# Performance work log

Measured on AMD Instinct MI355X. Metric: run time of the kernel, lower is better.

The kernel has to match this reference:

```python
import jax, jax.numpy as jnp
import numpy as np

N_STATE = 256   # complex state size n (real state is 2n)
N_IN = 128
BATCH = 16
T_STEPS = 2048
H_STEP = 0.01
EPS = 1e-3
LAM_RE_MIN, LAM_RE_MAX, MAX_PHASE = -5.0, -0.5, 6.283


def setup_inputs() -> dict:
    rng = np.random.default_rng(0)
    n, nu = N_STATE, N_IN
    # trainable params (as in torch __init__)
    u1 = rng.random(n)
    u2 = rng.random(n) * 2.0 - 1.0
    alpha = np.log(-(u1 * (LAM_RE_MAX - LAM_RE_MIN) + LAM_RE_MIN)).astype(np.float32)
    theta = (MAX_PHASE * u2).astype(np.float32)
    B_re = (rng.standard_normal((n, nu)) / np.sqrt(2.0 * nu)).astype(np.float32)
    B_im = (rng.standard_normal((n, nu)) / np.sqrt(2.0 * nu)).astype(np.float32)
    # fixed basis-change buffers: rho (normalized), T_inv, P = rho @ T_inv, Pinv
    H1 = rng.standard_normal((n, n))
    H2 = rng.standard_normal((n, n))
    rho = np.block([[H1, -H2], [H2, H1]])
    rho = rho / np.linalg.norm(rho)
    I = np.eye(n)
    T_inv = (1.0 / np.sqrt(2.0)) * np.block([[I, I], [-1j * I, 1j * I]])
    P = rho.astype(np.complex128) @ T_inv
    Pinv = np.linalg.inv(P)
    key = jax.random.key(0)
    k1, k2 = jax.random.split(key)
    return {
        "xi_init": jax.random.normal(k1, (BATCH, 1, 2 * n), dtype=jnp.float32),
        "u_log": jax.random.normal(k2, (BATCH, T_STEPS, nu), dtype=jnp.float32),
        "alpha": jnp.asarray(alpha),
        "theta": jnp.asarray(theta),
        "B_re": jnp.asarray(B_re),
        "B_im": jnp.asarray(B_im),
        "P_re": jnp.asarray(P.real, dtype=jnp.float32),
        "P_im": jnp.asarray(P.imag, dtype=jnp.float32),
        "Pinv_re": jnp.asarray(Pinv.real, dtype=jnp.float32),
        "Pinv_im": jnp.asarray(Pinv.imag, dtype=jnp.float32),
        "T": T_STEPS,
    }


def reference(xi_init, u_log, alpha, theta, B_re, B_im, P_re, P_im, Pinv_re, Pinv_im, T):
    n = alpha.shape[0]
    lam = (-jnp.exp(alpha) - EPS) + 1j * theta          # (n,) complex64
    Bc = B_re + 1j * B_im                               # (n, nu)
    P = P_re + 1j * P_im                                # (2n, 2n)
    Pinv = Pinv_re + 1j * Pinv_im                       # (2n, 2n)
    xi0 = xi_init[:, 0, :]                              # (B, 2n) real

    def step(xi, u_t):
        # xi: (B, 2n) real state; u_t: (B, nu)
        x_tilde = xi.astype(jnp.complex64) @ Pinv.T     # (B, 2n) complex
        x_bar = x_tilde[:, :n]                          # (B, n)
        x_bar_dot = lam * x_bar + u_t.astype(jnp.complex64) @ Bc.T
        x_tilde_dot = jnp.concatenate([x_bar_dot, jnp.conj(x_bar_dot)], axis=-1)
        x_dot = (x_tilde_dot @ P.T).real                # (B, 2n)
        xi_new = xi + H_STEP * x_dot
        return xi_new, xi_new

    u_seq = jnp.swapaxes(u_log, 0, 1)                   # (T, B, nu)
    _, xs = jax.lax.scan(step, xi0, u_seq)              # (T, B, 2n)
    # torch _sim logs xi_init, then skips xi after t=0, logs xi after t=1..T-1
    x_log = jnp.concatenate([xi0[None], xs[1:]], axis=0)  # (T, B, 2n)
    return jnp.swapaxes(x_log, 0, 1)                    # (B, T, 2n)
```

## Files before the change

kernel.cpp:

```cpp
#include <hip/hip_runtime.h>
#include <hip/hip_bf16.h>
#include <cstddef>
#include <cstdint>

#define N_ST 256
#define TWO_N 512
#define NU 128
#define BATCH 16
#define TSTEPS 2048
#define MTOT (BATCH * TSTEPS)
#define H_STEP 0.01f
#define EPS_V 0.001f
#define NCHUNK 32
#define CHUNKL 64

typedef __attribute__((ext_vector_type(4))) float f32x4;
typedef __attribute__((ext_vector_type(4))) short s16x4;
typedef __attribute__((ext_vector_type(8))) short s16x8;

#define OFF_FPK    0
#define OFF_ZPK    8388608
#define OFF_UPK    16777216
#define OFF_WT     18874368
#define OFF_WF     19005440
#define OFF_D      19038208
#define OFF_XBAR0  19039232
#define OFF_E      19047424

static __device__ __forceinline__ float bf2f(short s) {
    return __uint_as_float(((unsigned)(unsigned short)s) << 16);
}

__global__ __launch_bounds__(256) void prep_mega(
    const float* __restrict__ P_re, const float* __restrict__ P_im,
    const float* __restrict__ B_re, const float* __restrict__ B_im,
    const float* __restrict__ alpha, const float* __restrict__ theta,
    const float* __restrict__ Pinv_re, const float* __restrict__ Pinv_im,
    const float* __restrict__ xi0, const float* __restrict__ u,
    short* __restrict__ Wtpk, short* __restrict__ Wfpk,
    float* __restrict__ dbuf, float* __restrict__ xbar0,
    short* __restrict__ upk)
{
    __shared__ float xs[BATCH * TWO_N];
    int blk = blockIdx.x, tid = threadIdx.x;
    if (blk < 1024) {
        int idx = blk * 256 + tid;
        int j = idx >> 9, c = idx & 511;
        float v;
        if (c < N_ST) v = P_re[j * TWO_N + c] + P_re[j * TWO_N + c + N_ST];
        else          v = P_im[j * TWO_N + c] - P_im[j * TWO_N + c - N_ST];
        __hip_bfloat16 b = __float2bfloat16(v);
        Wtpk[((size_t)(j >> 4) * TWO_N + c) * 16 + (j & 15)] = *(short*)&b;
    } else if (blk < 1280) {
        int idx = (blk - 1024) * 256 + tid;
        int k = idx >> 9, c = idx & 511;
        float v = (c < N_ST) ? B_re[c * NU + k] : B_im[(c - N_ST) * NU + k];
        __hip_bfloat16 b = __float2bfloat16(H_STEP * v);
        Wfpk[((size_t)(c >> 4) * NU + k) * 16 + (c & 15)] = *(short*)&b;
    } else if (blk == 1280) {
        int i = tid;
        float dr = 1.0f + H_STEP * (-expf(alpha[i]) - EPS_V);
        float di = H_STEP * theta[i];
        float pr = 1.0f, pi = 0.0f;
        for (int k = 0; k < CHUNKL; ++k) { float nr = pr * dr - pi * di; pi = pr * di + pi * dr; pr = nr; }
        dbuf[i] = dr; dbuf[N_ST + i] = di; dbuf[2 * N_ST + i] = pr; dbuf[3 * N_ST + i] = pi;
    } else if (blk < 1345) {
#pragma unroll
        for (int q = 0; q < 8; ++q)
            *reinterpret_cast<float4*>(&xs[(q * 256 + tid) * 4]) =
                *reinterpret_cast<const float4*>(&xi0[(q * 256 + tid) * 4]);
        __syncthreads();
        int wv = tid >> 6, l = tid & 63;
        int i = (blk - 1281) * 4 + wv;
        float rp[BATCH] = {}, ip[BATCH] = {};
#pragma unroll
        for (int q = 0; q < 8; ++q) {
            int j = q * 64 + l;
            float pr = Pinv_re[(size_t)i * TWO_N + j];
            float pi = Pinv_im[(size_t)i * TWO_N + j];
#pragma unroll
            for (int b = 0; b < BATCH; ++b) {
                float x = xs[b * TWO_N + j];
                rp[b] = fmaf(pr, x, rp[b]);
                ip[b] = fmaf(pi, x, ip[b]);
            }
        }
#pragma unroll
        for (int m = 1; m < 64; m <<= 1) {
#pragma unroll
            for (int b = 0; b < BATCH; ++b) {
                rp[b] += __shfl_xor(rp[b], m, 64);
                ip[b] += __shfl_xor(ip[b], m, 64);
            }
        }
        if (l == 0) {
#pragma unroll
            for (int b = 0; b < BATCH; ++b) {
                xbar0[b * TWO_N + i] = rp[b];
                xbar0[b * TWO_N + N_ST + i] = ip[b];
            }
        }
    } else {
        short* st = (short*)xs;
        int bid = blk - 1345;
        const float* up = u + (size_t)bid * 8192;
#pragma unroll
        for (int q = 0; q < 8; ++q) {
            int idx = q * 1024 + tid * 4;
            float4 v = *reinterpret_cast<const float4*>(up + idx);
            int m = idx >> 7, k = idx & 127;
            s16x4 pv;
            __hip_bfloat16 b0 = __float2bfloat16(v.x); pv[0] = *(short*)&b0;
            __hip_bfloat16 b1 = __float2bfloat16(v.y); pv[1] = *(short*)&b1;
            __hip_bfloat16 b2 = __float2bfloat16(v.z); pv[2] = *(short*)&b2;
            __hip_bfloat16 b3 = __float2bfloat16(v.w); pv[3] = *(short*)&b3;
            *reinterpret_cast<__shared__ s16x4*>(&st[m * 132 + k]) = pv;
        }
        __syncthreads();
        short* op = upk + (size_t)bid * 8192;
#pragma unroll
        for (int q2 = 0; q2 < 4; ++q2) {
            int o = q2 * 2048 + tid * 8;
            int ml = o & 15, k = (o >> 4) & 127, sl = o >> 11;
            s16x8 w;
#pragma unroll
            for (int r = 0; r < 8; ++r) w[r] = st[(sl * 16 + ml + r) * 132 + k];
            *reinterpret_cast<s16x8*>(op + o) = w;
        }
    }
}

template <int K, bool PACKOUT>
__global__ __launch_bounds__(512, 4) void gemm_mfma(const short* __restrict__ Apk,
                                                    const short* __restrict__ Bpk,
                                                    float* __restrict__ Cf,
                                                    short* __restrict__ Cp,
                                                    const float* __restrict__ xi0) {
    __shared__ __align__(1024) short lds[36864];
    const int tid = threadIdx.x;
    const int wid = tid >> 6, lane = tid & 63;
    const int l = blockIdx.x;
    const int mb = ((l >> 4) << 3) | (l & 7);
    const int nb = (l >> 3) & 1;
    const int m0 = mb * 128, n0 = nb * 256;
    const int wm = wid >> 2, wn = wid & 3;
    f32x4 acc[4][4] = {};
    const size_t slabStride = (size_t)K * 16;
    const unsigned ldsBase = (unsigned)(uintptr_t)(__attribute__((address_space(3))) short*)&lds[0];
    constexpr int NT = K / 32;

#define STAGE(buf, kk)                                                                              \
    do {                                                                                            \
        _Pragma("unroll")                                                                           \
        for (int q_ = 0; q_ < 3; ++q_) {                                                            \
            int s_ = wid + q_ * 8;                                                                  \
            const short* src_ = (s_ < 8 ? Apk + ((size_t)(m0 >> 4) + s_) * slabStride               \
                                        : Bpk + ((size_t)(n0 >> 4) + (s_ - 8)) * slabStride)        \
                                + (size_t)(kk) * 16 + lane * 8;                                     \
            __builtin_amdgcn_global_load_lds((const __attribute__((address_space(1))) void*)src_,   \
                (__attribute__((address_space(3))) void*)&lds[(buf) * 12288 + s_ * 512], 16, 0, 0); \
        }                                                                                           \
    } while (0)

    STAGE(0, 0);
    STAGE(1, 32);

#pragma unroll
    for (int t = 0; t < NT; ++t) {
        const int cur = t % 3;
        if (t + 2 < NT) STAGE((t + 2) % 3, (t + 2) * 32);

        if (t + 2 < NT)      asm volatile("s_waitcnt vmcnt(6)" ::: "memory");
        else if (t + 1 < NT) asm volatile("s_waitcnt vmcnt(3)" ::: "memory");
        else                 asm volatile("s_waitcnt vmcnt(0)" ::: "memory");
        __builtin_amdgcn_sched_barrier(0);
        __builtin_amdgcn_s_barrier();
        __builtin_amdgcn_sched_barrier(0);

        s16x4 al[4], ah[4], bl[4], bh[4];
        const unsigned base_ = ldsBase + (unsigned)cur * 24576u;
#pragma unroll
        for (int i = 0; i < 4; ++i) {
            unsigned ad = base_ + ((unsigned)(wm * 4 + i) << 10) + ((unsigned)lane << 3);
            asm volatile("ds_read_b64_tr_b16 %0, %1 offset:0"   : "=v"(al[i]) : "v"(ad));
            asm volatile("ds_read_b64_tr_b16 %0, %1 offset:512" : "=v"(ah[i]) : "v"(ad));
        }
#pragma unroll
        for (int j = 0; j < 4; ++j) {
            unsigned bd = base_ + ((unsigned)(8 + wn * 4 + j) << 10) + ((unsigned)lane << 3);
            asm volatile("ds_read_b64_tr_b16 %0, %1 offset:0"   : "=v"(bl[j]) : "v"(bd));
            asm volatile("ds_read_b64_tr_b16 %0, %1 offset:512" : "=v"(bh[j]) : "v"(bd));
        }
        asm volatile("s_waitcnt lgkmcnt(0)" ::: "memory");
        __builtin_amdgcn_sched_barrier(0);
        __builtin_amdgcn_s_barrier();
        __builtin_amdgcn_sched_barrier(0);

        __builtin_amdgcn_s_setprio(1);
#pragma unroll
        for (int i = 0; i < 4; ++i) {
            s16x8 av = __builtin_shufflevector(al[i], ah[i], 0, 1, 2, 3, 4, 5, 6, 7);
#pragma unroll
            for (int j = 0; j < 4; ++j) {
                s16x8 bv = __builtin_shufflevector(bl[j], bh[j], 0, 1, 2, 3, 4, 5, 6, 7);
                acc[i][j] = __builtin_amdgcn_mfma_f32_16x16x32_bf16(av, bv, acc[i][j], 0, 0, 0);
            }
        }
        __builtin_amdgcn_s_setprio(0);
    }
#undef STAGE

    const int cn = lane & 15;
    const int g4 = (lane >> 4) * 4;
    if (!PACKOUT) {
#pragma unroll
        for (int i = 0; i < 4; ++i) {
            int mrow = m0 + wm * 64 + i * 16 + g4;
#pragma unroll
            for (int j = 0; j < 4; ++j) {
                int ncol = n0 + wn * 64 + j * 16 + cn;
                float* cp = Cf + (size_t)mrow * TWO_N + ncol;
#pragma unroll
                for (int r = 0; r < 4; ++r) {
                    float v = acc[i][j][r];
                    if (((mrow + r) & (TSTEPS - 1)) == 0)
                        v = xi0[((mrow + r) >> 11) * TWO_N + ncol];
                    cp[(size_t)r * TWO_N] = v;
                }
            }
        }
    } else {
#pragma unroll
        for (int i = 0; i < 4; ++i) {
            size_t slab = (size_t)((m0 >> 4) + wm * 4 + i);
#pragma unroll
            for (int j = 0; j < 4; ++j) {
                int n = n0 + wn * 64 + j * 16 + cn;
                s16x4 pv;
#pragma unroll
                for (int r = 0; r < 4; ++r) {
                    __hip_bfloat16 bb = __float2bfloat16(acc[i][j][r]);
                    pv[r] = *reinterpret_cast<short*>(&bb);
                }
                *reinterpret_cast<s16x4*>(Cp + slab * 8192 + (size_t)n * 16 + g4) = pv;
            }
        }
    }
}

__global__ __launch_bounds__(256) void scan_passA(const short* __restrict__ Fpk,
                                                  const float* __restrict__ dbuf,
                                                  float* __restrict__ e) {
    int b = blockIdx.x, c = blockIdx.y, i = threadIdx.x;
    float dr = dbuf[i], di = dbuf[N_ST + i];
    float re = 0.f, im = 0.f;
    int slab0 = (b * TSTEPS + c * CHUNKL) >> 4;
#pragma unroll
    for (int g = 0; g < 4; ++g) {
        const short* base = Fpk + (size_t)(slab0 + g) * 8192 + i * 16;
        s16x8 r0 = *reinterpret_cast<const s16x8*>(base);
        s16x8 r1 = *reinterpret_cast<const s16x8*>(base + 8);
        s16x8 i0 = *reinterpret_cast<const s16x8*>(base + 4096);
        s16x8 i1 = *reinterpret_cast<const s16x8*>(base + 4096 + 8);
#pragma unroll
        for (int j = 0; j < 16; ++j) {
            float fr = bf2f(j < 8 ? r0[j & 7] : r1[j & 7]);
            float fi = bf2f(j < 8 ? i0[j & 7] : i1[j & 7]);
            float nre = fmaf(dr, re, fmaf(-di, im, fr));
            float nim = fmaf(dr, im, fmaf(di, re, fi));
            re = nre; im = nim;
        }
    }
    size_t o = ((size_t)(b * NCHUNK + c)) * TWO_N;
    e[o + i] = re;
    e[o + N_ST + i] = im;
}

__global__ __launch_bounds__(256) void scan_passC(const short* __restrict__ Fpk,
                                                  const float* __restrict__ dbuf,
                                                  const float* __restrict__ e,
                                                  const float* __restrict__ xbar0,
                                                  short* __restrict__ Zpk) {
    int b = blockIdx.x, c = blockIdx.y, i = threadIdx.x;
    float dr = dbuf[i], di = dbuf[N_ST + i];
    float dLr = dbuf[2 * N_ST + i], dLi = dbuf[3 * N_ST + i];
    float re = xbar0[b * TWO_N + i], im = xbar0[b * TWO_N + N_ST + i];
    for (int cc = 0; cc < c; ++cc) {
        size_t o = ((size_t)(b * NCHUNK + cc)) * TWO_N;
        float er = e[o + i], ei = e[o + N_ST + i];
        float nre = fmaf(dLr, re, fmaf(-dLi, im, er));
        float nim = fmaf(dLr, im, fmaf(dLi, re, ei));
        re = nre; im = nim;
    }
    int slab0 = (b * TSTEPS + c * CHUNKL) >> 4;
#pragma unroll
    for (int g = 0; g < 4; ++g) {
        const short* base = Fpk + (size_t)(slab0 + g) * 8192 + i * 16;
        s16x8 r0 = *reinterpret_cast<const s16x8*>(base);
        s16x8 r1 = *reinterpret_cast<const s16x8*>(base + 8);
        s16x8 i0 = *reinterpret_cast<const s16x8*>(base + 4096);
        s16x8 i1 = *reinterpret_cast<const s16x8*>(base + 4096 + 8);
        s16x8 zr0, zr1, zi0, zi1;
#pragma unroll
        for (int j = 0; j < 16; ++j) {
            float fr = bf2f(j < 8 ? r0[j & 7] : r1[j & 7]);
            float fi = bf2f(j < 8 ? i0[j & 7] : i1[j & 7]);
            float nre = fmaf(dr, re, fmaf(-di, im, fr));
            float nim = fmaf(dr, im, fmaf(di, re, fi));
            re = nre; im = nim;
            __hip_bfloat16 br = __float2bfloat16(re), bi = __float2bfloat16(im);
            if (j < 8) { zr0[j & 7] = *(short*)&br; zi0[j & 7] = *(short*)&bi; }
            else       { zr1[j & 7] = *(short*)&br; zi1[j & 7] = *(short*)&bi; }
        }
        short* zb = Zpk + (size_t)(slab0 + g) * 8192 + i * 16;
        *reinterpret_cast<s16x8*>(zb)            = zr0;
        *reinterpret_cast<s16x8*>(zb + 8)        = zr1;
        *reinterpret_cast<s16x8*>(zb + 4096)     = zi0;
        *reinterpret_cast<s16x8*>(zb + 4096 + 8) = zi1;
    }
}

extern "C" void kernel_launch(void* const* d_in, const int* in_sizes, int n_in,
                              void* d_out, int out_size, void* d_ws, size_t ws_size,
                              hipStream_t stream) {
    const float* xi_init = (const float*)d_in[0];
    const float* u_log   = (const float*)d_in[1];
    const float* alpha   = (const float*)d_in[2];
    const float* theta   = (const float*)d_in[3];
    const float* B_re    = (const float*)d_in[4];
    const float* B_im    = (const float*)d_in[5];
    const float* P_re    = (const float*)d_in[6];
    const float* P_im    = (const float*)d_in[7];
    const float* Pinv_re = (const float*)d_in[8];
    const float* Pinv_im = (const float*)d_in[9];
    float* out = (float*)d_out;
    float* ws  = (float*)d_ws;

    short* Fpk  = (short*)(ws + OFF_FPK);
    short* Zpk  = (short*)(ws + OFF_ZPK);
    short* upk  = (short*)(ws + OFF_UPK);
    short* Wtpk = (short*)(ws + OFF_WT);
    short* Wfpk = (short*)(ws + OFF_WF);
    float* dbuf  = ws + OFF_D;
    float* xbar0 = ws + OFF_XBAR0;
    float* e     = ws + OFF_E;

    prep_mega<<<1857, 256, 0, stream>>>(P_re, P_im, B_re, B_im, alpha, theta,
                                        Pinv_re, Pinv_im, xi_init, u_log,
                                        Wtpk, Wfpk, dbuf, xbar0, upk);

    gemm_mfma<NU, true><<<512, 512, 0, stream>>>(
        upk, Wfpk, nullptr, Fpk, nullptr);

    scan_passA<<<dim3(BATCH, NCHUNK), 256, 0, stream>>>(Fpk, dbuf, e);
    scan_passC<<<dim3(BATCH, NCHUNK), 256, 0, stream>>>(Fpk, dbuf, e, xbar0, Zpk);

    gemm_mfma<TWO_N, false><<<512, 512, 0, stream>>>(
        Zpk, Wtpk, out, nullptr, xi_init);
}
```

Measured before the change: 74.76 us.

## Fuse input GEMM, chunked scan and output GEMM into per-chunk kernels

Replaces the separate input-projection GEMM, the two scan passes and the output GEMM with one chunk kernel, launched twice. The first launch computes the chunk end states and the second recomputes the input projection, runs the scan in LDS with the chunk's initial state and applies the output projection. A small sequential pass B supplies the chunk initial states, so the quadratic per-chunk prefix loop of the old pass C goes away. This removes the global round-trips of the Fpk and Zpk intermediates at the cost of computing the input GEMM twice. It also gives each block a 64-row tile that runs a serial 64-step scan on half of its threads.

```diff
diff --git a/kernel.cpp b/kernel.cpp
--- a/kernel.cpp
+++ b/kernel.cpp
@@ -13,22 +13,33 @@
 #define EPS_V 0.001f
 #define NCHUNK 32
 #define CHUNKL 64
+#define NBLK (MTOT / CHUNKL)
 
 typedef __attribute__((ext_vector_type(4))) float f32x4;
 typedef __attribute__((ext_vector_type(4))) short s16x4;
 typedef __attribute__((ext_vector_type(8))) short s16x8;
 
-#define OFF_FPK    0
-#define OFF_ZPK    8388608
-#define OFF_UPK    16777216
-#define OFF_WT     18874368
-#define OFF_WF     19005440
-#define OFF_D      19038208
-#define OFF_XBAR0  19039232
-#define OFF_E      19047424
+#define AS1 __attribute__((address_space(1)))
+#define AS3 __attribute__((address_space(3)))
+
+#define OFF_UPK    0
+#define OFF_WT     2097152
+#define OFF_WF     2228224
+#define OFF_D      2260992
+#define OFF_XBAR0  2262016
+#define OFF_E      2270208
+#define OFF_CINIT  2532352
+
+#define F_B 0
+#define B_B 65536
+#define U_B 131072
 
 static __device__ __forceinline__ float bf2f(short s) {
     return __uint_as_float(((unsigned)(unsigned short)s) << 16);
+}
+static __device__ __forceinline__ short f2bf(float f) {
+    __hip_bfloat16 b = __float2bfloat16(f);
+    return *reinterpret_cast<short*>(&b);
 }
 
 __global__ __launch_bounds__(256) void prep_mega(
@@ -49,14 +60,12 @@
         float v;
         if (c < N_ST) v = P_re[j * TWO_N + c] + P_re[j * TWO_N + c + N_ST];
         else          v = P_im[j * TWO_N + c] - P_im[j * TWO_N + c - N_ST];
-        __hip_bfloat16 b = __float2bfloat16(v);
-        Wtpk[((size_t)(j >> 4) * TWO_N + c) * 16 + (j & 15)] = *(short*)&b;
+        Wtpk[((size_t)(j >> 4) * TWO_N + c) * 16 + (j & 15)] = f2bf(v);
     } else if (blk < 1280) {
         int idx = (blk - 1024) * 256 + tid;
         int k = idx >> 9, c = idx & 511;
         float v = (c < N_ST) ? B_re[c * NU + k] : B_im[(c - N_ST) * NU + k];
-        __hip_bfloat16 b = __float2bfloat16(H_STEP * v);
-        Wfpk[((size_t)(c >> 4) * NU + k) * 16 + (c & 15)] = *(short*)&b;
+        Wfpk[((size_t)(c >> 4) * NU + k) * 16 + (c & 15)] = f2bf(H_STEP * v);
     } else if (blk == 1280) {
         int i = tid;
         float dr = 1.0f + H_STEP * (-expf(alpha[i]) - EPS_V);
@@ -110,10 +119,7 @@
             float4 v = *reinterpret_cast<const float4*>(up + idx);
             int m = idx >> 7, k = idx & 127;
             s16x4 pv;
-            __hip_bfloat16 b0 = __float2bfloat16(v.x); pv[0] = *(short*)&b0;
-            __hip_bfloat16 b1 = __float2bfloat16(v.y); pv[1] = *(short*)&b1;
-            __hip_bfloat16 b2 = __float2bfloat16(v.z); pv[2] = *(short*)&b2;
-            __hip_bfloat16 b3 = __float2bfloat16(v.w); pv[3] = *(short*)&b3;
+            pv[0] = f2bf(v.x); pv[1] = f2bf(v.y); pv[2] = f2bf(v.z); pv[3] = f2bf(v.w);
             *reinterpret_cast<__shared__ s16x4*>(&st[m * 132 + k]) = pv;
         }
         __syncthreads();
@@ -130,64 +136,63 @@
     }
 }
 
-template <int K, bool PACKOUT>
-__global__ __launch_bounds__(512, 4) void gemm_mfma(const short* __restrict__ Apk,
-                                                    const short* __restrict__ Bpk,
-                                                    float* __restrict__ Cf,
-                                                    short* __restrict__ Cp,
-                                                    const float* __restrict__ xi0) {
-    __shared__ __align__(1024) short lds[36864];
+template <bool FULL>
+__global__ __launch_bounds__(512, 2) void chunk_kernel(
+    const short* __restrict__ upk, const short* __restrict__ Wfpk,
+    const short* __restrict__ Wtpk, const float* __restrict__ dbuf,
+    const float* __restrict__ cinit, float* __restrict__ e,
+    const float* __restrict__ xi0, float* __restrict__ out)
+{
+    __shared__ __align__(1024) short lds[73728];
+    char* smem = (char*)lds;
     const int tid = threadIdx.x;
-    const int wid = tid >> 6, lane = tid & 63;
-    const int l = blockIdx.x;
-    const int mb = ((l >> 4) << 3) | (l & 7);
-    const int nb = (l >> 3) & 1;
-    const int m0 = mb * 128, n0 = nb * 256;
-    const int wm = wid >> 2, wn = wid & 3;
-    f32x4 acc[4][4] = {};
-    const size_t slabStride = (size_t)K * 16;
-    const unsigned ldsBase = (unsigned)(uintptr_t)(__attribute__((address_space(3))) short*)&lds[0];
-    constexpr int NT = K / 32;
-
-#define STAGE(buf, kk)                                                                              \
+    const int w = tid >> 6, lane = tid & 63;
+    const int laneL = lane & 15, laneH = lane >> 4;
+    const int cid = blockIdx.x;
+    const unsigned ldsA = (unsigned)(uintptr_t)(AS3 short*)&lds[0];
+
+    {
+        const short* usrc = upk + (size_t)(cid * 4) * 2048;
+#pragma unroll
+        for (int q = 0; q < 2; ++q) {
+            int c_ = w * 2 + q;
+            __builtin_amdgcn_global_load_lds((const AS1 void*)(usrc + c_ * 512 + lane * 8),
+                (AS3 void*)(smem + U_B + c_ * 1024), 16, 0, 0);
+        }
+    }
+#define STAGE_B(Wsrc, slabStrideShorts, buf, kk)                                                    \
     do {                                                                                            \
         _Pragma("unroll")                                                                           \
-        for (int q_ = 0; q_ < 3; ++q_) {                                                            \
-            int s_ = wid + q_ * 8;                                                                  \
-            const short* src_ = (s_ < 8 ? Apk + ((size_t)(m0 >> 4) + s_) * slabStride               \
-                                        : Bpk + ((size_t)(n0 >> 4) + (s_ - 8)) * slabStride)        \
-                                + (size_t)(kk) * 16 + lane * 8;                                     \
-            __builtin_amdgcn_global_load_lds((const __attribute__((address_space(1))) void*)src_,   \
-                (__attribute__((address_space(3))) void*)&lds[(buf) * 12288 + s_ * 512], 16, 0, 0); \
+        for (int q_ = 0; q_ < 4; ++q_) {                                                            \
+            int s_ = w + q_ * 8;                                                                    \
+            __builtin_amdgcn_global_load_lds(                                                       \
+                (const AS1 void*)((Wsrc) + (size_t)s_ * (slabStrideShorts) + (size_t)(kk) * 16 + lane * 8), \
+                (AS3 void*)(smem + B_B + (buf) * 32768 + s_ * 1024), 16, 0, 0);                     \
         }                                                                                           \
     } while (0)
 
-    STAGE(0, 0);
-    STAGE(1, 32);
-
-#pragma unroll
-    for (int t = 0; t < NT; ++t) {
-        const int cur = t % 3;
-        if (t + 2 < NT) STAGE((t + 2) % 3, (t + 2) * 32);
-
-        if (t + 2 < NT)      asm volatile("s_waitcnt vmcnt(6)" ::: "memory");
-        else if (t + 1 < NT) asm volatile("s_waitcnt vmcnt(3)" ::: "memory");
-        else                 asm volatile("s_waitcnt vmcnt(0)" ::: "memory");
+    f32x4 acc[4][4] = {};
+    STAGE_B(Wfpk, 2048, 0, 0);
+#pragma unroll
+    for (int t = 0; t < 4; ++t) {
+        const int buf = t & 1;
+        if (t + 1 < 4) STAGE_B(Wfpk, 2048, buf ^ 1, (t + 1) * 32);
+        if (t + 1 < 4) asm volatile("s_waitcnt vmcnt(4)" ::: "memory");
+        else           asm volatile("s_waitcnt vmcnt(0)" ::: "memory");
         __builtin_amdgcn_sched_barrier(0);
         __builtin_amdgcn_s_barrier();
         __builtin_amdgcn_sched_barrier(0);
 
         s16x4 al[4], ah[4], bl[4], bh[4];
-        const unsigned base_ = ldsBase + (unsigned)cur * 24576u;
 #pragma unroll
         for (int i = 0; i < 4; ++i) {
-            unsigned ad = base_ + ((unsigned)(wm * 4 + i) << 10) + ((unsigned)lane << 3);
+            unsigned ad = ldsA + U_B + (unsigned)i * 4096u + (unsigned)t * 1024u + ((unsigned)lane << 3);
             asm volatile("ds_read_b64_tr_b16 %0, %1 offset:0"   : "=v"(al[i]) : "v"(ad));
             asm volatile("ds_read_b64_tr_b16 %0, %1 offset:512" : "=v"(ah[i]) : "v"(ad));
         }
 #pragma unroll
         for (int j = 0; j < 4; ++j) {
-            unsigned bd = base_ + ((unsigned)(8 + wn * 4 + j) << 10) + ((unsigned)lane << 3);
+            unsigned bd = ldsA + B_B + (unsigned)buf * 32768u + ((unsigned)(w * 4 + j) << 10) + ((unsigned)lane << 3);
             asm volatile("ds_read_b64_tr_b16 %0, %1 offset:0"   : "=v"(bl[j]) : "v"(bd));
             asm volatile("ds_read_b64_tr_b16 %0, %1 offset:512" : "=v"(bh[j]) : "v"(bd));
         }
@@ -208,115 +213,126 @@
         }
         __builtin_amdgcn_s_setprio(0);
     }
-#undef STAGE
-
-    const int cn = lane & 15;
-    const int g4 = (lane >> 4) * 4;
-    if (!PACKOUT) {
-#pragma unroll
-        for (int i = 0; i < 4; ++i) {
-            int mrow = m0 + wm * 64 + i * 16 + g4;
-#pragma unroll
-            for (int j = 0; j < 4; ++j) {
-                int ncol = n0 + wn * 64 + j * 16 + cn;
-                float* cp = Cf + (size_t)mrow * TWO_N + ncol;
-#pragma unroll
-                for (int r = 0; r < 4; ++r) {
-                    float v = acc[i][j][r];
-                    if (((mrow + r) & (TSTEPS - 1)) == 0)
-                        v = xi0[((mrow + r) >> 11) * TWO_N + ncol];
-                    cp[(size_t)r * TWO_N] = v;
-                }
-            }
-        }
-    } else {
-#pragma unroll
-        for (int i = 0; i < 4; ++i) {
-            size_t slab = (size_t)((m0 >> 4) + wm * 4 + i);
-#pragma unroll
-            for (int j = 0; j < 4; ++j) {
-                int n = n0 + wn * 64 + j * 16 + cn;
-                s16x4 pv;
-#pragma unroll
-                for (int r = 0; r < 4; ++r) {
-                    __hip_bfloat16 bb = __float2bfloat16(acc[i][j][r]);
-                    pv[r] = *reinterpret_cast<short*>(&bb);
-                }
-                *reinterpret_cast<s16x4*>(Cp + slab * 8192 + (size_t)n * 16 + g4) = pv;
-            }
-        }
-    }
-}
-
-__global__ __launch_bounds__(256) void scan_passA(const short* __restrict__ Fpk,
-                                                  const float* __restrict__ dbuf,
-                                                  float* __restrict__ e) {
-    int b = blockIdx.x, c = blockIdx.y, i = threadIdx.x;
-    float dr = dbuf[i], di = dbuf[N_ST + i];
-    float re = 0.f, im = 0.f;
-    int slab0 = (b * TSTEPS + c * CHUNKL) >> 4;
-#pragma unroll
-    for (int g = 0; g < 4; ++g) {
-        const short* base = Fpk + (size_t)(slab0 + g) * 8192 + i * 16;
-        s16x8 r0 = *reinterpret_cast<const s16x8*>(base);
-        s16x8 r1 = *reinterpret_cast<const s16x8*>(base + 8);
-        s16x8 i0 = *reinterpret_cast<const s16x8*>(base + 4096);
-        s16x8 i1 = *reinterpret_cast<const s16x8*>(base + 4096 + 8);
-#pragma unroll
-        for (int j = 0; j < 16; ++j) {
-            float fr = bf2f(j < 8 ? r0[j & 7] : r1[j & 7]);
-            float fi = bf2f(j < 8 ? i0[j & 7] : i1[j & 7]);
+#pragma unroll
+    for (int i = 0; i < 4; ++i) {
+#pragma unroll
+        for (int j = 0; j < 4; ++j) {
+            int s = w * 64 + j * 16 + laneL;
+#pragma unroll
+            for (int r = 0; r < 4; ++r) {
+                int t = i * 16 + laneH * 4 + r;
+                *(short*)(smem + F_B + t * 1024 + (((unsigned)(2 * s)) ^ (unsigned)((t & 15) << 3))) =
+                    f2bf(acc[i][j][r]);
+            }
+        }
+    }
+    __syncthreads();
+
+    if (FULL) STAGE_B(Wtpk, 8192, 0, 0);
+
+    if (tid < 256) {
+        const int i2 = tid;
+        float dr = dbuf[i2], di = dbuf[N_ST + i2];
+        float re, im;
+        if (FULL) { re = cinit[(size_t)cid * TWO_N + i2]; im = cinit[(size_t)cid * TWO_N + N_ST + i2]; }
+        else      { re = 0.f; im = 0.f; }
+        const unsigned colr = (unsigned)(2 * i2);
+#pragma unroll 8
+        for (int t = 0; t < CHUNKL; ++t) {
+            char* p = smem + F_B + t * 1024 + (colr ^ (unsigned)((t & 15) << 3));
+            float fr = bf2f(*(short*)p);
+            float fi = bf2f(*(short*)(p + 512));
             float nre = fmaf(dr, re, fmaf(-di, im, fr));
             float nim = fmaf(dr, im, fmaf(di, re, fi));
             re = nre; im = nim;
-        }
-    }
-    size_t o = ((size_t)(b * NCHUNK + c)) * TWO_N;
-    e[o + i] = re;
-    e[o + N_ST + i] = im;
-}
-
-__global__ __launch_bounds__(256) void scan_passC(const short* __restrict__ Fpk,
-                                                  const float* __restrict__ dbuf,
-                                                  const float* __restrict__ e,
-                                                  const float* __restrict__ xbar0,
-                                                  short* __restrict__ Zpk) {
-    int b = blockIdx.x, c = blockIdx.y, i = threadIdx.x;
-    float dr = dbuf[i], di = dbuf[N_ST + i];
+            if (FULL) { *(short*)p = f2bf(re); *(short*)(p + 512) = f2bf(im); }
+        }
+        if (!FULL) {
+            e[(size_t)cid * TWO_N + i2] = re;
+            e[(size_t)cid * TWO_N + N_ST + i2] = im;
+        }
+    }
+    if (!FULL) return;
+    __syncthreads();
+
+    f32x4 acc2[4][4] = {};
+#pragma unroll
+    for (int t = 0; t < 16; ++t) {
+        const int buf = t & 1;
+        if (t + 1 < 16) STAGE_B(Wtpk, 8192, buf ^ 1, (t + 1) * 32);
+        if (t + 1 < 16) asm volatile("s_waitcnt vmcnt(4)" ::: "memory");
+        else            asm volatile("s_waitcnt vmcnt(0)" ::: "memory");
+        __builtin_amdgcn_sched_barrier(0);
+        __builtin_amdgcn_s_barrier();
+        __builtin_amdgcn_sched_barrier(0);
+
+        s16x8 av[4];
+        {
+            const unsigned klo = (unsigned)((t * 32 + laneH * 4) * 2);
+            const unsigned swz = (unsigned)(laneL << 3);
+#pragma unroll
+            for (int i = 0; i < 4; ++i) {
+                char* base = smem + F_B + (i * 16 + laneL) * 1024;
+                s16x4 lo = *(const s16x4*)(base + (klo ^ swz));
+                s16x4 hi = *(const s16x4*)(base + ((klo + 32) ^ swz));
+                av[i] = __builtin_shufflevector(lo, hi, 0, 1, 2, 3, 4, 5, 6, 7);
+            }
+        }
+        s16x4 bl[4], bh[4];
+#pragma unroll
+        for (int j = 0; j < 4; ++j) {
+            unsigned bd = ldsA + B_B + (unsigned)buf * 32768u + ((unsigned)(w * 4 + j) << 10) + ((unsigned)lane << 3);
+            asm volatile("ds_read_b64_tr_b16 %0, %1 offset:0"   : "=v"(bl[j]) : "v"(bd));
+            asm volatile("ds_read_b64_tr_b16 %0, %1 offset:512" : "=v"(bh[j]) : "v"(bd));
+        }
+        asm volatile("s_waitcnt lgkmcnt(0)" ::: "memory");
+        __builtin_amdgcn_sched_barrier(0);
+        __builtin_amdgcn_s_barrier();
+        __builtin_amdgcn_sched_barrier(0);
+
+        __builtin_amdgcn_s_setprio(1);
+#pragma unroll
+        for (int j = 0; j < 4; ++j) {
+            s16x8 bv = __builtin_shufflevector(bl[j], bh[j], 0, 1, 2, 3, 4, 5, 6, 7);
+#pragma unroll
+            for (int i = 0; i < 4; ++i)
+                acc2[i][j] = __builtin_amdgcn_mfma_f32_16x16x32_bf16(av[i], bv, acc2[i][j], 0, 0, 0);
+        }
+        __builtin_amdgcn_s_setprio(0);
+    }
+#undef STAGE_B
+
+#pragma unroll
+    for (int i = 0; i < 4; ++i) {
+        int mrow = cid * 64 + i * 16 + laneH * 4;
+#pragma unroll
+        for (int j = 0; j < 4; ++j) {
+            int ncol = w * 64 + j * 16 + laneL;
+            float* cp = out + (size_t)mrow * TWO_N + ncol;
+#pragma unroll
+            for (int r = 0; r < 4; ++r) {
+                float v = acc2[i][j][r];
+                if (((mrow + r) & (TSTEPS - 1)) == 0)
+                    v = xi0[((mrow + r) >> 11) * TWO_N + ncol];
+                cp[(size_t)r * TWO_N] = v;
+            }
+        }
+    }
+}
+
+__global__ void scan_passB(const float* __restrict__ e, const float* __restrict__ dbuf,
+                           const float* __restrict__ xbar0, float* __restrict__ cinit) {
+    int b = blockIdx.x, i = threadIdx.x;
     float dLr = dbuf[2 * N_ST + i], dLi = dbuf[3 * N_ST + i];
     float re = xbar0[b * TWO_N + i], im = xbar0[b * TWO_N + N_ST + i];
-    for (int cc = 0; cc < c; ++cc) {
-        size_t o = ((size_t)(b * NCHUNK + cc)) * TWO_N;
+    for (int c = 0; c < NCHUNK; ++c) {
+        size_t o = ((size_t)(b * NCHUNK + c)) * TWO_N;
+        cinit[o + i] = re;
+        cinit[o + N_ST + i] = im;
         float er = e[o + i], ei = e[o + N_ST + i];
         float nre = fmaf(dLr, re, fmaf(-dLi, im, er));
         float nim = fmaf(dLr, im, fmaf(dLi, re, ei));
         re = nre; im = nim;
-    }
-    int slab0 = (b * TSTEPS + c * CHUNKL) >> 4;
-#pragma unroll
-    for (int g = 0; g < 4; ++g) {
-        const short* base = Fpk + (size_t)(slab0 + g) * 8192 + i * 16;
-        s16x8 r0 = *reinterpret_cast<const s16x8*>(base);
-        s16x8 r1 = *reinterpret_cast<const s16x8*>(base + 8);
-        s16x8 i0 = *reinterpret_cast<const s16x8*>(base + 4096);
-        s16x8 i1 = *reinterpret_cast<const s16x8*>(base + 4096 + 8);
-        s16x8 zr0, zr1, zi0, zi1;
-#pragma unroll
-        for (int j = 0; j < 16; ++j) {
-            float fr = bf2f(j < 8 ? r0[j & 7] : r1[j & 7]);
-            float fi = bf2f(j < 8 ? i0[j & 7] : i1[j & 7]);
-            float nre = fmaf(dr, re, fmaf(-di, im, fr));
-            float nim = fmaf(dr, im, fmaf(di, re, fi));
-            re = nre; im = nim;
-            __hip_bfloat16 br = __float2bfloat16(re), bi = __float2bfloat16(im);
-            if (j < 8) { zr0[j & 7] = *(short*)&br; zi0[j & 7] = *(short*)&bi; }
-            else       { zr1[j & 7] = *(short*)&br; zi1[j & 7] = *(short*)&bi; }
-        }
-        short* zb = Zpk + (size_t)(slab0 + g) * 8192 + i * 16;
-        *reinterpret_cast<s16x8*>(zb)            = zr0;
-        *reinterpret_cast<s16x8*>(zb + 8)        = zr1;
-        *reinterpret_cast<s16x8*>(zb + 4096)     = zi0;
-        *reinterpret_cast<s16x8*>(zb + 4096 + 8) = zi1;
     }
 }
 
@@ -336,25 +352,23 @@
     float* out = (float*)d_out;
     float* ws  = (float*)d_ws;
 
-    short* Fpk  = (short*)(ws + OFF_FPK);
-    short* Zpk  = (short*)(ws + OFF_ZPK);
     short* upk  = (short*)(ws + OFF_UPK);
     short* Wtpk = (short*)(ws + OFF_WT);
     short* Wfpk = (short*)(ws + OFF_WF);
     float* dbuf  = ws + OFF_D;
     float* xbar0 = ws + OFF_XBAR0;
     float* e     = ws + OFF_E;
+    float* cinit = ws + OFF_CINIT;
 
     prep_mega<<<1857, 256, 0, stream>>>(P_re, P_im, B_re, B_im, alpha, theta,
                                         Pinv_re, Pinv_im, xi_init, u_log,
                                         Wtpk, Wfpk, dbuf, xbar0, upk);
 
-    gemm_mfma<NU, true><<<512, 512, 0, stream>>>(
-        upk, Wfpk, nullptr, Fpk, nullptr);
-
-    scan_passA<<<dim3(BATCH, NCHUNK), 256, 0, stream>>>(Fpk, dbuf, e);
-    scan_passC<<<dim3(BATCH, NCHUNK), 256, 0, stream>>>(Fpk, dbuf, e, xbar0, Zpk);
-
-    gemm_mfma<TWO_N, false><<<512, 512, 0, stream>>>(
-        Zpk, Wtpk, out, nullptr, xi_init);
-}
+    chunk_kernel<false><<<NBLK, 512, 0, stream>>>(
+        upk, Wfpk, Wtpk, dbuf, nullptr, e, nullptr, nullptr);
+
+    scan_passB<<<BATCH, 256, 0, stream>>>(e, dbuf, xbar0, cinit);
+
+    chunk_kernel<true><<<NBLK, 512, 0, stream>>>(
+        upk, Wfpk, Wtpk, dbuf, cinit, nullptr, xi_init, out);
+}
```

After: 83.25 us. 11.4% more time.
